# Performance work log

Measured on AMD Instinct MI355X. Metric: run time of the kernel, lower is better.

## Reference

```python
import jax, jax.numpy as jnp
import numpy as np

B, S, D, H = 4, 1024, 1024, 16
DEPTH = D // H


def setup_inputs() -> dict:
    key = jax.random.key(0)
    ks = jax.random.split(key, 13)
    inp = {
        'query': jax.random.normal(ks[0], (B, S, D), dtype=jnp.float32),
        'key': jax.random.normal(ks[1], (B, S, D), dtype=jnp.float32),
        'value': jax.random.normal(ks[2], (B, S, D), dtype=jnp.float32),
        'mask': jax.random.bernoulli(ks[3], 0.1, (B, S, S)),
    }
    scale = 1.0 / np.sqrt(D)
    inp['wq_w'] = jax.random.uniform(ks[4], (D, D), jnp.float32, -scale, scale)
    inp['wq_b'] = jax.random.uniform(ks[5], (D,), jnp.float32, -scale, scale)
    inp['wk_w'] = jax.random.uniform(ks[6], (D, D), jnp.float32, -scale, scale)
    inp['wk_b'] = jax.random.uniform(ks[7], (D,), jnp.float32, -scale, scale)
    inp['wv_w'] = jax.random.uniform(ks[8], (D, D), jnp.float32, -scale, scale)
    inp['wv_b'] = jax.random.uniform(ks[9], (D,), jnp.float32, -scale, scale)
    inp['fc_w'] = jax.random.uniform(ks[10], (D, D), jnp.float32, -scale, scale)
    inp['fc_b'] = jax.random.uniform(ks[11], (D,), jnp.float32, -scale, scale)
    return inp


def _split_heads(x):
    # [B,S,D] -> [B,H,S,depth]
    b, s, _ = x.shape
    return x.reshape(b, s, H, DEPTH).transpose(0, 2, 1, 3)


def reference(query, key, value, mask, wq_w, wq_b, wk_w, wk_b, wv_w, wv_b, fc_w, fc_b):
    q = _split_heads(query @ wq_w.T + wq_b)
    k = _split_heads(key @ wk_w.T + wk_b)
    v = _split_heads(value @ wv_w.T + wv_b)
    scores = jnp.einsum('bhqd,bhkd->bhqk', q, k) / jnp.sqrt(jnp.float32(DEPTH))
    scores = jnp.where(mask[:, None, :, :], jnp.float32(-1e9), scores)
    attn = jax.nn.softmax(scores, axis=-1)
    out = jnp.einsum('bhqk,bhkd->bhqd', attn, v)  # [B,H,S,depth]
    out = out.transpose(0, 2, 1, 3).reshape(query.shape[0], -1, D)
    return out @ fc_w.T + fc_b
```

## Files before the change

### kernel.cpp

```cpp
#include <hip/hip_runtime.h>
#include <hip/hip_bf16.h>


typedef __bf16 bf16x8 __attribute__((ext_vector_type(8)));
typedef __bf16 bf16x4 __attribute__((ext_vector_type(4)));
typedef float  f32x4  __attribute__((ext_vector_type(4)));
typedef float  f32x16 __attribute__((ext_vector_type(16)));

typedef const __attribute__((address_space(1))) void* gptr_t;
typedef __attribute__((address_space(3))) void* lptr_t;

#define MFMA16(a, b, c) __builtin_amdgcn_mfma_f32_16x16x32_bf16((a), (b), (c), 0, 0, 0)
#define MFMA32(a, b, c) __builtin_amdgcn_mfma_f32_32x32x16_bf16((a), (b), (c), 0, 0, 0)

__device__ __forceinline__ void gload_lds16(const void* g, void* l) {
  __builtin_amdgcn_global_load_lds((gptr_t)g, (lptr_t)l, 16, 0, 0);
}

__device__ __forceinline__ unsigned pack2(float a, float b) {
  union { __bf16 h[2]; unsigned u; } x;
  x.h[0] = (__bf16)a; x.h[1] = (__bf16)b; return x.u;
}

__device__ __forceinline__ bf16x8 mkfrag(unsigned a, unsigned b, unsigned c, unsigned d) {
  union { unsigned w[4]; bf16x8 v; } x;
  x.w[0] = a; x.w[1] = b; x.w[2] = c; x.w[3] = d; return x.v;
}

__global__ void detect_mask(const unsigned char* m, int* flag) {
  __shared__ int s1[4], s23[4];
  int tid = threadIdx.x;
  uint4 v = ((const uint4*)m)[tid];
  unsigned x0 = v.x, x1 = v.y, x2 = v.z, x3 = v.w;
  unsigned c1  = (x0 & 0x0000ff00u) | (x1 & 0x0000ff00u) | (x2 & 0x0000ff00u) | (x3 & 0x0000ff00u);
  unsigned c23 = (x0 & 0xffff0000u) | (x1 & 0xffff0000u) | (x2 & 0xffff0000u) | (x3 & 0xffff0000u);
  unsigned long long b1 = __ballot(c1 != 0), b23 = __ballot(c23 != 0);
  if ((tid & 63) == 0) { s1[tid >> 6] = (b1 != 0); s23[tid >> 6] = (b23 != 0); }
  __syncthreads();
  if (tid == 0) {
    int a1 = s1[0] | s1[1] | s1[2] | s1[3];
    int a23 = s23[0] | s23[1] | s23[2] | s23[3];
    *flag = a1 ? 1 : (a23 ? 2 : 0);
  }
}

__global__ void pack_mask(const void* m, const int* flag, unsigned int* out) {
  size_t i = (size_t)blockIdx.x * 256 + threadIdx.x;
  int f = *flag;
  bool v;
  if (f == 1)      v = ((const unsigned char*)m)[i] != 0;
  else if (f == 2) v = ((const float*)m)[i] != 0.0f;
  else             v = ((const int*)m)[i] != 0;
  unsigned long long bal = __ballot(v);
  int lane = threadIdx.x & 63;
  if ((lane & 31) == 0) out[i >> 5] = (unsigned int)(bal >> (lane & 32));
}

__global__ void cvt_all(const float* q, const float* k, const float* v,
                        const float* w0, const float* w1, const float* w2, const float* w3,
                        __bf16* oq, __bf16* ok, __bf16* ov,
                        __bf16* o0, __bf16* o1, __bf16* o2, __bf16* o3) {
  int bid = blockIdx.x;
  const float* in; __bf16* out; int sub;
  if (bid < 12288) {
    int w = bid >> 12; sub = bid & 4095;
    in = w == 0 ? q : w == 1 ? k : v;
    out = w == 0 ? oq : w == 1 ? ok : ov;
  } else {
    int w = (bid - 12288) >> 10; sub = (bid - 12288) & 1023;
    in = w == 0 ? w0 : w == 1 ? w1 : w == 2 ? w2 : w3;
    out = w == 0 ? o0 : w == 1 ? o1 : w == 2 ? o2 : o3;
  }
  size_t i = (size_t)sub * 256 + threadIdx.x;
  float4 vv = ((const float4*)in)[i];
  bf16x4 o; o[0] = (__bf16)vv.x; o[1] = (__bf16)vv.y; o[2] = (__bf16)vv.z; o[3] = (__bf16)vv.w;
  ((bf16x4*)out)[i] = o;
}

__global__ __launch_bounds__(256, 2)
void gemm_qkv(const __bf16* __restrict__ qb, const __bf16* __restrict__ kb,
              const __bf16* __restrict__ vb,
              const __bf16* __restrict__ wq, const __bf16* __restrict__ wk,
              const __bf16* __restrict__ wv,
              const float* __restrict__ bq, const float* __restrict__ bk,
              const float* __restrict__ bv,
              __bf16* __restrict__ Qp, __bf16* __restrict__ Kp, __bf16* __restrict__ Vt) {
  __shared__ __bf16 As[2][128 * 64];
  __shared__ __bf16 Bs[2][128 * 64];
  const int bm = blockIdx.x;
  const int bnall = blockIdx.y;
  const int which = bnall >> 3;
  const int bn = bnall & 7;
  const __bf16* A = which == 0 ? qb : which == 1 ? kb : vb;
  const __bf16* W = which == 0 ? wq : which == 1 ? wk : wv;
  const float* bias = which == 0 ? bq : which == 1 ? bk : bv;

  const int tid = threadIdx.x, wave = tid >> 6, lane = tid & 63;
  const int wr = wave >> 1, wc = wave & 1;
  const int rl = lane >> 3, c8 = lane & 7;
  f32x4 acc[4][4] = {};

#define QKV_STAGE(bb, kt)                                                             \
  {                                                                                   \
    _Pragma("unroll")                                                                 \
    for (int i = 0; i < 4; ++i) {                                                     \
      int row = wave * 32 + i * 8 + rl;                                               \
      int sw = (c8 ^ (row & 7)) << 3;                                                 \
      gload_lds16(A + (size_t)(bm * 128 + row) * 1024 + (kt) * 64 + sw,               \
                  &As[bb][(wave * 32 + i * 8) * 64]);                                 \
      gload_lds16(W + (size_t)(bn * 128 + row) * 1024 + (kt) * 64 + sw,               \
                  &Bs[bb][(wave * 32 + i * 8) * 64]);                                 \
    }                                                                                 \
  }

  QKV_STAGE(0, 0);
  __syncthreads();
  int buf = 0;
  for (int kt = 0; kt < 16; ++kt) {
    if (kt < 15) QKV_STAGE(buf ^ 1, kt + 1);
#pragma unroll
    for (int k32 = 0; k32 < 2; ++k32) {
      bf16x8 af[4], bfr[4];
#pragma unroll
      for (int mi = 0; mi < 4; ++mi) {
        int row = wr * 64 + mi * 16 + (lane & 15);
        af[mi] = *(const bf16x8*)(&As[buf][row * 64 + (((k32 * 4 + (lane >> 4)) ^ (row & 7)) << 3)]);
      }
#pragma unroll
      for (int ni = 0; ni < 4; ++ni) {
        int row = wc * 64 + ni * 16 + (lane & 15);
        bfr[ni] = *(const bf16x8*)(&Bs[buf][row * 64 + (((k32 * 4 + (lane >> 4)) ^ (row & 7)) << 3)]);
      }
#pragma unroll
      for (int mi = 0; mi < 4; ++mi)
#pragma unroll
        for (int ni = 0; ni < 4; ++ni)
          acc[mi][ni] = MFMA16(af[mi], bfr[ni], acc[mi][ni]);
    }
    __syncthreads();
    buf ^= 1;
  }
  const int r0 = (lane >> 4) * 4, cl = lane & 15;
  __bf16* Onat = which == 0 ? Qp : Kp;
#pragma unroll
  for (int ni = 0; ni < 4; ++ni) {
    int col = bn * 128 + wc * 64 + ni * 16 + cl;
    float bvv = bias[col];
#pragma unroll
    for (int mi = 0; mi < 4; ++mi) {
      int rowb = bm * 128 + wr * 64 + mi * 16 + r0;
      if (which < 2) {
#pragma unroll
        for (int r = 0; r < 4; ++r)
          Onat[(size_t)(rowb + r) * 1024 + col] = (__bf16)(acc[mi][ni][r] + bvv);
      } else {
        int bb = rowb >> 10, s0 = rowb & 1023, hh = col >> 6, d = col & 63;
        bf16x4 ov;
#pragma unroll
        for (int r = 0; r < 4; ++r) ov[r] = (__bf16)(acc[mi][ni][r] + bvv);
        *(bf16x4*)(Vt + (((size_t)(bb * 16 + hh) * 64 + d) << 10) + s0) = ov;
      }
    }
  }
}

__global__ __launch_bounds__(256, 2)
void gemm_fc(const __bf16* __restrict__ A, const __bf16* __restrict__ W,
             const float* __restrict__ bias, float* __restrict__ C) {
  __shared__ __bf16 As[2][128 * 64];
  __shared__ __bf16 Bs[2][128 * 64];
  const int bm = blockIdx.x, bn = blockIdx.y;
  const int tid = threadIdx.x, wave = tid >> 6, lane = tid & 63;
  const int wr = wave >> 1, wc = wave & 1;
  const int rl = lane >> 3, c8 = lane & 7;
  f32x4 acc[4][4] = {};

#define FC_STAGE(bb, kt)                                                              \
  {                                                                                   \
    _Pragma("unroll")                                                                 \
    for (int i = 0; i < 4; ++i) {                                                     \
      int row = wave * 32 + i * 8 + rl;                                               \
      int sw = (c8 ^ (row & 7)) << 3;                                                 \
      gload_lds16(A + (size_t)(bm * 128 + row) * 1024 + (kt) * 64 + sw,               \
                  &As[bb][(wave * 32 + i * 8) * 64]);                                 \
      gload_lds16(W + (size_t)(bn * 128 + row) * 1024 + (kt) * 64 + sw,               \
                  &Bs[bb][(wave * 32 + i * 8) * 64]);                                 \
    }                                                                                 \
  }

  FC_STAGE(0, 0);
  __syncthreads();
  int buf = 0;
  for (int kt = 0; kt < 16; ++kt) {
    if (kt < 15) FC_STAGE(buf ^ 1, kt + 1);
#pragma unroll
    for (int k32 = 0; k32 < 2; ++k32) {
      bf16x8 af[4], bfr[4];
#pragma unroll
      for (int mi = 0; mi < 4; ++mi) {
        int row = wr * 64 + mi * 16 + (lane & 15);
        af[mi] = *(const bf16x8*)(&As[buf][row * 64 + (((k32 * 4 + (lane >> 4)) ^ (row & 7)) << 3)]);
      }
#pragma unroll
      for (int ni = 0; ni < 4; ++ni) {
        int row = wc * 64 + ni * 16 + (lane & 15);
        bfr[ni] = *(const bf16x8*)(&Bs[buf][row * 64 + (((k32 * 4 + (lane >> 4)) ^ (row & 7)) << 3)]);
      }
#pragma unroll
      for (int mi = 0; mi < 4; ++mi)
#pragma unroll
        for (int ni = 0; ni < 4; ++ni)
          acc[mi][ni] = MFMA16(af[mi], bfr[ni], acc[mi][ni]);
    }
    __syncthreads();
    buf ^= 1;
  }
  const int r0 = (lane >> 4) * 4, cl = lane & 15;
#pragma unroll
  for (int ni = 0; ni < 4; ++ni) {
    int col = bn * 128 + wc * 64 + ni * 16 + cl;
    float bvv = bias[col];
#pragma unroll
    for (int mi = 0; mi < 4; ++mi) {
      int rowb = bm * 128 + wr * 64 + mi * 16 + r0;
#pragma unroll
      for (int r = 0; r < 4; ++r)
        C[(size_t)(rowb + r) * 1024 + col] = acc[mi][ni][r] + bvv;
    }
  }
}

__global__ __launch_bounds__(256)
void attn32(const __bf16* __restrict__ Qp, const __bf16* __restrict__ Kp,
            const __bf16* __restrict__ Vt, const unsigned long long* __restrict__ mp64,
            __bf16* __restrict__ O) {
  __shared__ __bf16 Ks[2][64 * 64];
  __shared__ __bf16 Vs[2][64 * 64];
  const int tid = threadIdx.x, wave = tid >> 6, lane = tid & 63;
  const int lo5 = lane & 31, hi = lane >> 5;
  const int bx = blockIdx.x;
  const int qt = bx & 7, h = (bx >> 3) & 15, b = bx >> 7;
  const int qrow = qt * 128 + wave * 32 + lo5;
  const float SC = 0.18033688011112042f;

  const int srow = tid >> 3;
  const int sgx = ((tid & 7) ^ (srow & 7)) << 3;

#define ATTN_STAGE(bb, kt)                                                            \
  {                                                                                   \
    _Pragma("unroll")                                                                 \
    for (int i = 0; i < 2; ++i) {                                                     \
      gload_lds16(Kp + (size_t)(b * 1024 + (kt) * 64 + i * 32 + srow) * 1024          \
                     + h * 64 + sgx,                                                  \
                  &Ks[bb][i * 2048 + wave * 512]);                                    \
      gload_lds16(Vt + (size_t)((b * 16 + h) * 64 + i * 32 + srow) * 1024             \
                     + (kt) * 64 + sgx,                                               \
                  &Vs[bb][i * 2048 + wave * 512]);                                    \
    }                                                                                 \
  }

  bf16x8 qf[4];
  const __bf16* qb = Qp + ((size_t)(b * 1024 + qrow)) * 1024 + h * 64 + hi * 8;
#pragma unroll
  for (int m = 0; m < 4; ++m) qf[m] = *(const bf16x8*)(qb + m * 16);

  f32x16 oacc0 = {}, oacc1 = {};
  float dsum = 0.0f;
  const unsigned long long* mrow = mp64 + ((size_t)(b * 1024 + qrow)) * 16;
  const int x = lo5 & 7;

  ATTN_STAGE(0, 0);
  __syncthreads();
  int buf = 0;
  for (int kt = 0; kt < 16; ++kt) {
    if (kt < 15) ATTN_STAGE(buf ^ 1, kt + 1);
    unsigned long long mw = mrow[kt];
#pragma unroll
    for (int sub = 0; sub < 2; ++sub) {
      f32x16 s = {};
#pragma unroll
      for (int m = 0; m < 4; ++m) {
        bf16x8 kf = *(const bf16x8*)(&Ks[buf][(sub * 32 + lo5) * 64 + (((2 * m + hi) ^ x) << 3)]);
        s = MFMA32(kf, qf[m], s);
      }
      float p[16];
#pragma unroll
      for (int r = 0; r < 16; ++r) {
        int cr = (r & 3) + 8 * (r >> 2) + 4 * hi;
        float e = exp2f(s[r] * SC);
        p[r] = ((mw >> (sub * 32 + cr)) & 1) ? 0.0f : e;
        dsum += p[r];
      }
      unsigned own[8], rcv[8];
#pragma unroll
      for (int u = 0; u < 4; ++u) {
        own[2 * u]     = pack2(p[4 * u],     p[4 * u + 1]);
        own[2 * u + 1] = pack2(p[4 * u + 2], p[4 * u + 3]);
      }
#pragma unroll
      for (int i = 0; i < 8; ++i) rcv[i] = (unsigned)__shfl_xor((int)own[i], 32, 64);
#pragma unroll
      for (int sf = 0; sf < 2; ++sf) {
        const int ue2 = 4 * sf, uo2 = 4 * sf + 2;
        unsigned fw0 = hi ? rcv[uo2 + 0] : own[ue2 + 0];
        unsigned fw1 = hi ? rcv[uo2 + 1] : own[ue2 + 1];
        unsigned fw2 = hi ? own[uo2 + 0] : rcv[ue2 + 0];
        unsigned fw3 = hi ? own[uo2 + 1] : rcv[ue2 + 1];
        bf16x8 pa = mkfrag(fw0, fw1, fw2, fw3);
        int g = ((sub * 4 + sf * 2 + hi) ^ x) << 3;
        bf16x8 vf0 = *(const bf16x8*)(&Vs[buf][lo5 * 64 + g]);
        bf16x8 vf1 = *(const bf16x8*)(&Vs[buf][(lo5 + 32) * 64 + g]);
        oacc0 = MFMA32(pa, vf0, oacc0);
        oacc1 = MFMA32(pa, vf1, oacc1);
      }
    }
    __syncthreads();
    buf ^= 1;
  }

  dsum += __shfl_xor(dsum, 32, 64);
  float inv = 1.0f / dsum;

  const size_t orow0 = (size_t)(b * 1024 + qt * 128 + wave * 32);
#pragma unroll
  for (int r = 0; r < 16; ++r) {
    int cr = (r & 3) + 8 * (r >> 2) + 4 * hi;
    float iv = __shfl(inv, cr, 64);
    __bf16* op = O + (orow0 + cr) * 1024 + h * 64 + lo5;
    op[0]  = (__bf16)(oacc0[r] * iv);
    op[32] = (__bf16)(oacc1[r] * iv);
  }
}

extern "C" void kernel_launch(void* const* d_in, const int* in_sizes, int n_in,
                              void* d_out, int out_size, void* d_ws, size_t ws_size,
                              hipStream_t stream) {
  const float* query = (const float*)d_in[0];
  const float* key   = (const float*)d_in[1];
  const float* value = (const float*)d_in[2];
  const void*  mask  = d_in[3];
  const float* wq_w  = (const float*)d_in[4];
  const float* wq_b  = (const float*)d_in[5];
  const float* wk_w  = (const float*)d_in[6];
  const float* wk_b  = (const float*)d_in[7];
  const float* wv_w  = (const float*)d_in[8];
  const float* wv_b  = (const float*)d_in[9];
  const float* fc_w  = (const float*)d_in[10];
  const float* fc_b  = (const float*)d_in[11];

  char* ws = (char*)d_ws;
  __bf16* qb  = (__bf16*)ws;
  __bf16* kb  = qb  + 4194304;
  __bf16* vb  = kb  + 4194304;
  __bf16* wqb = vb  + 4194304;
  __bf16* wkb = wqb + 1048576;
  __bf16* wvb = wkb + 1048576;
  __bf16* fcb = wvb + 1048576;
  __bf16* Qp  = fcb + 1048576;
  __bf16* Kp  = Qp  + 4194304;
  __bf16* Vt  = Kp  + 4194304;
  __bf16* Ob  = Vt  + 4194304;
  unsigned int* mpk = (unsigned int*)(Ob + 4194304);
  int* flag = (int*)(mpk + 131072);

  detect_mask<<<1, 256, 0, stream>>>((const unsigned char*)mask, flag);
  pack_mask<<<16384, 256, 0, stream>>>(mask, flag, mpk);
  cvt_all<<<16384, 256, 0, stream>>>(query, key, value, wq_w, wk_w, wv_w, fc_w,
                                     qb, kb, vb, wqb, wkb, wvb, fcb);
  dim3 g1(32, 24);
  gemm_qkv<<<g1, 256, 0, stream>>>(qb, kb, vb, wqb, wkb, wvb, wq_b, wk_b, wv_b, Qp, Kp, Vt);
  attn32<<<512, 256, 0, stream>>>(Qp, Kp, Vt, (const unsigned long long*)mpk, Ob);
  dim3 g2(32, 8);
  gemm_fc<<<g2, 256, 0, stream>>>(Ob, fcb, fc_b, (float*)d_out);
}
```

Baseline: 248.3 us.

## Fold softmax scale into Q projection and compute row sums via MFMA

Folds the softmax scale (1/sqrt(depth) times log2 e) into the Q projection epilogue so attention uses raw hardware exp2. The mask test becomes a bitfield-extract AND, and the mask word for the next tile is prefetched one iteration early. Cross-lane shuffles for P fragments are replaced by v_permlane32_swap. The scalar denominator accumulation is replaced by an extra MFMA against a ones vector, so the row sum comes from bf16-rounded probabilities. This trades VALU and shuffle work for one extra MFMA per fragment and slightly different rounding.

Result: faster. 236.6 us (-4.7%).

```diff
diff --git a/kernel.cpp b/kernel.cpp
--- a/kernel.cpp
+++ b/kernel.cpp
@@ -141,6 +141,7 @@
     buf ^= 1;
   }
   const int r0 = (lane >> 4) * 4, cl = lane & 15;
+  const float osc = (which == 0) ? 0.18033688011112042f : 1.0f;
   __bf16* Onat = which == 0 ? Qp : Kp;
 #pragma unroll
   for (int ni = 0; ni < 4; ++ni) {
@@ -152,7 +153,7 @@
       if (which < 2) {
 #pragma unroll
         for (int r = 0; r < 4; ++r)
-          Onat[(size_t)(rowb + r) * 1024 + col] = (__bf16)(acc[mi][ni][r] + bvv);
+          Onat[(size_t)(rowb + r) * 1024 + col] = (__bf16)((acc[mi][ni][r] + bvv) * osc);
       } else {
         int bb = rowb >> 10, s0 = rowb & 1023, hh = col >> 6, d = col & 63;
         bf16x4 ov;
@@ -232,7 +233,7 @@
 
 __global__ __launch_bounds__(256)
 void attn32(const __bf16* __restrict__ Qp, const __bf16* __restrict__ Kp,
-            const __bf16* __restrict__ Vt, const unsigned long long* __restrict__ mp64,
+            const __bf16* __restrict__ Vt, const unsigned int* __restrict__ mp,
             __bf16* __restrict__ O) {
   __shared__ __bf16 Ks[2][64 * 64];
   __shared__ __bf16 Vs[2][64 * 64];
@@ -241,7 +242,6 @@
   const int bx = blockIdx.x;
   const int qt = bx & 7, h = (bx >> 3) & 15, b = bx >> 7;
   const int qrow = qt * 128 + wave * 32 + lo5;
-  const float SC = 0.18033688011112042f;
 
   const int srow = tid >> 3;
   const int sgx = ((tid & 7) ^ (srow & 7)) << 3;
@@ -264,17 +264,22 @@
 #pragma unroll
   for (int m = 0; m < 4; ++m) qf[m] = *(const bf16x8*)(qb + m * 16);
 
-  f32x16 oacc0 = {}, oacc1 = {};
-  float dsum = 0.0f;
-  const unsigned long long* mrow = mp64 + ((size_t)(b * 1024 + qrow)) * 16;
+  bf16x8 onesf;
+#pragma unroll
+  for (int i = 0; i < 8; ++i) onesf[i] = (__bf16)1.0f;
+
+  f32x16 oacc0 = {}, oacc1 = {}, oaccD = {};
+  const uint2* mrow = ((const uint2*)mp) + ((size_t)(b * 1024 + qrow)) * 16;
   const int x = lo5 & 7;
 
   ATTN_STAGE(0, 0);
+  uint2 mwc = mrow[0];
   __syncthreads();
   int buf = 0;
   for (int kt = 0; kt < 16; ++kt) {
     if (kt < 15) ATTN_STAGE(buf ^ 1, kt + 1);
-    unsigned long long mw = mrow[kt];
+    uint2 mwn = mwc;
+    if (kt < 15) mwn = mrow[kt + 1];
 #pragma unroll
     for (int sub = 0; sub < 2; ++sub) {
       f32x16 s = {};
@@ -283,49 +288,46 @@
         bf16x8 kf = *(const bf16x8*)(&Ks[buf][(sub * 32 + lo5) * 64 + (((2 * m + hi) ^ x) << 3)]);
         s = MFMA32(kf, qf[m], s);
       }
+      unsigned w32 = sub == 0 ? mwc.x : mwc.y;
+      unsigned nw = ~(w32 >> (hi * 4));
       float p[16];
 #pragma unroll
       for (int r = 0; r < 16; ++r) {
-        int cr = (r & 3) + 8 * (r >> 2) + 4 * hi;
-        float e = exp2f(s[r] * SC);
-        p[r] = ((mw >> (sub * 32 + cr)) & 1) ? 0.0f : e;
-        dsum += p[r];
-      }
-      unsigned own[8], rcv[8];
+        float e = __builtin_amdgcn_exp2f(s[r]);
+        unsigned keep = (unsigned)__builtin_amdgcn_sbfe((int)nw, (unsigned)((r & 3) + 8 * (r >> 2)), 1u);
+        p[r] = __uint_as_float(__float_as_uint(e) & keep);
+      }
+      unsigned own[8];
 #pragma unroll
       for (int u = 0; u < 4; ++u) {
         own[2 * u]     = pack2(p[4 * u],     p[4 * u + 1]);
         own[2 * u + 1] = pack2(p[4 * u + 2], p[4 * u + 3]);
       }
 #pragma unroll
-      for (int i = 0; i < 8; ++i) rcv[i] = (unsigned)__shfl_xor((int)own[i], 32, 64);
-#pragma unroll
       for (int sf = 0; sf < 2; ++sf) {
-        const int ue2 = 4 * sf, uo2 = 4 * sf + 2;
-        unsigned fw0 = hi ? rcv[uo2 + 0] : own[ue2 + 0];
-        unsigned fw1 = hi ? rcv[uo2 + 1] : own[ue2 + 1];
-        unsigned fw2 = hi ? own[uo2 + 0] : rcv[ue2 + 0];
-        unsigned fw3 = hi ? own[uo2 + 1] : rcv[ue2 + 1];
-        bf16x8 pa = mkfrag(fw0, fw1, fw2, fw3);
+        unsigned a0 = own[4 * sf + 0], b0 = own[4 * sf + 2];
+        unsigned a1 = own[4 * sf + 1], b1 = own[4 * sf + 3];
+        asm volatile("v_permlane32_swap_b32 %0, %1" : "+v"(a0), "+v"(b0));
+        asm volatile("v_permlane32_swap_b32 %0, %1" : "+v"(a1), "+v"(b1));
+        bf16x8 pa = mkfrag(a0, a1, b0, b1);
         int g = ((sub * 4 + sf * 2 + hi) ^ x) << 3;
         bf16x8 vf0 = *(const bf16x8*)(&Vs[buf][lo5 * 64 + g]);
         bf16x8 vf1 = *(const bf16x8*)(&Vs[buf][(lo5 + 32) * 64 + g]);
         oacc0 = MFMA32(pa, vf0, oacc0);
         oacc1 = MFMA32(pa, vf1, oacc1);
+        oaccD = MFMA32(pa, onesf, oaccD);
       }
     }
     __syncthreads();
     buf ^= 1;
-  }
-
-  dsum += __shfl_xor(dsum, 32, 64);
-  float inv = 1.0f / dsum;
+    mwc = mwn;
+  }
 
   const size_t orow0 = (size_t)(b * 1024 + qt * 128 + wave * 32);
 #pragma unroll
   for (int r = 0; r < 16; ++r) {
     int cr = (r & 3) + 8 * (r >> 2) + 4 * hi;
-    float iv = __shfl(inv, cr, 64);
+    float iv = __builtin_amdgcn_rcpf(oaccD[r]);
     __bf16* op = O + (orow0 + cr) * 1024 + h * 64 + lo5;
     op[0]  = (__bf16)(oacc0[r] * iv);
     op[32] = (__bf16)(oacc1[r] * iv);
@@ -369,7 +371,7 @@
                                      qb, kb, vb, wqb, wkb, wvb, fcb);
   dim3 g1(32, 24);
   gemm_qkv<<<g1, 256, 0, stream>>>(qb, kb, vb, wqb, wkb, wvb, wq_b, wk_b, wv_b, Qp, Kp, Vt);
-  attn32<<<512, 256, 0, stream>>>(Qp, Kp, Vt, (const unsigned long long*)mpk, Ob);
+  attn32<<<512, 256, 0, stream>>>(Qp, Kp, Vt, mpk, Ob);
   dim3 g2(32, 8);
   gemm_fc<<<g2, 256, 0, stream>>>(Ob, fcb, fc_b, (float*)d_out);
 }
```
